# Performance work log

Hardware: AMD Instinct MI355X
Metric: run time of the kernel (lower is better)

Reference implementation:

```python
import jax, jax.numpy as jnp
import numpy as np

N_NODES = 50000
N_EDGES = 600000
N_REL = 8
D_IN = 128
D_OUT = 128


def setup_inputs() -> dict:
    key = jax.random.key(0)
    ks = jax.random.split(key, 12)
    s = 1.0 / np.sqrt(D_IN)
    s2 = 1.0 / np.sqrt(2 * D_IN)
    return {
        "x": jax.random.normal(ks[0], (N_NODES, D_IN), jnp.float32),
        "src": jax.random.randint(ks[1], (N_EDGES,), 0, N_NODES, jnp.int32),
        "dst": jax.random.randint(ks[2], (N_EDGES,), 0, N_NODES, jnp.int32),
        "etype": jax.random.randint(ks[3], (N_EDGES,), 0, N_REL, jnp.int32),
        "Wrel": jax.random.normal(ks[4], (N_REL, D_IN, D_OUT), jnp.float32) * s,
        "Wloop": jax.random.normal(ks[5], (D_IN, D_OUT), jnp.float32) * s,
        "brel": jax.random.normal(ks[6], (D_OUT,), jnp.float32) * s,
        "W1": jax.random.normal(ks[7], (2 * D_IN, 2 * D_IN), jnp.float32) * s2,
        "b1": jax.random.normal(ks[8], (2 * D_IN,), jnp.float32) * s2,
        "W2": jax.random.normal(ks[9], (2 * D_IN, D_OUT), jnp.float32) * s2,
        "b2": jax.random.normal(ks[10], (D_OUT,), jnp.float32) * s2,
    }


def rel_graph_conv(x, src, dst, etype, Wrel, Wloop, brel):
    # low_mem style: transform node features once per relation, then gather per edge.
    xW = jnp.einsum('ni,rio->rno', x, Wrel)          # [R, N, D_OUT]
    msg = xW[etype, src]                              # [E, D_OUT] gather by (rel, src)
    agg = jax.ops.segment_sum(msg, dst, num_segments=N_NODES)  # scatter-add to dst
    return agg + x @ Wloop + brel                     # self-loop + bias (DGL defaults)


def reference(x, src, dst, etype, Wrel, Wloop, brel, W1, b1, W2, b2):
    mid = rel_graph_conv(x, src, dst, etype, Wrel, Wloop, brel)
    h = jnp.concatenate([x, mid], axis=1)             # [N, 2*D_IN]
    h = jax.nn.relu(h @ W1 + b1)
    return h @ W2 + b2
```

## Files before the change

### kernel.cpp

```cpp
#include <hip/hip_runtime.h>

#define N_NODES 50000
#define N_EDGES 600000
#define N_REL 8
#define NT_PAD 50176
#define N_TILES 196

typedef __attribute__((ext_vector_type(8))) short bf16x8;
typedef __attribute__((ext_vector_type(4))) float f32x4;

__device__ __forceinline__ ushort f2b(float f) {
    union { float f; unsigned u; } v; v.f = f;
    unsigned r = v.u + 0x7FFFu + ((v.u >> 16) & 1u);
    return (ushort)(r >> 16);
}
__device__ __forceinline__ float b2f(ushort s) {
    union { unsigned u; float f; } v; v.u = ((unsigned)s) << 16;
    return v.f;
}


__global__ void conv_f32_bf16(const float* __restrict__ in, ushort* __restrict__ outb) {
    int i = (blockIdx.x * 256 + threadIdx.x) * 4;
    float4 f = *(const float4*)(in + i);
    ushort4 o; o.x = f2b(f.x); o.y = f2b(f.y); o.z = f2b(f.z); o.w = f2b(f.w);
    *(ushort4*)(outb + i) = o;
}

__global__ void transpose_wts3(const float* __restrict__ Wloop, const float* __restrict__ Wrel,
                               const float* __restrict__ W1, const float* __restrict__ W2,
                               ushort* __restrict__ wt) {
    int y = blockIdx.y;
    if (y == 0) {
        for (int idx = blockIdx.x * 256 + threadIdx.x; idx < 128 * 1152; idx += gridDim.x * 256) {
            int c = idx / 1152, kg = idx - c * 1152;
            float v = (kg < 1024) ? Wrel[(size_t)((kg >> 7) * 128 + (kg & 127)) * 128 + c]
                                  : Wloop[(size_t)(kg - 1024) * 128 + c];
            wt[idx] = f2b(v);
        }
    } else if (y == 1) {
        for (int idx = blockIdx.x * 256 + threadIdx.x; idx < 256 * 256; idx += gridDim.x * 256) {
            int c = idx >> 8, k = idx & 255;
            wt[147456 + idx] = f2b(W1[k * 256 + c]);
        }
    } else {
        for (int idx = blockIdx.x * 256 + threadIdx.x; idx < 128 * 256; idx += gridDim.x * 256) {
            int c = idx >> 8, k = idx & 255;
            wt[212992 + idx] = f2b(W2[k * 128 + c]);
        }
    }
}

template<int NPH, int KMODE, int AS, int CTOT, int OMODE>
__global__ __launch_bounds__(256) void mfma_gemm(
        const ushort* __restrict__ A0, const ushort* __restrict__ A1,
        const ushort* __restrict__ Bt, const float* __restrict__ bias,
        void* __restrict__ outv) {
    __shared__ ushort bs[128 * 136];
    const int t = threadIdx.x;
    const int wave = t >> 6, lane = t & 63;
    const int lr = lane & 15, lg = lane >> 4;
    const int wr = (wave >> 1) * 64, wc = (wave & 1) * 64;
    const int row0 = blockIdx.x * 128;
    const ushort* Btb = Bt + (size_t)blockIdx.y * 128 * (NPH * 128);

    f32x4 acc[4][4];
#pragma unroll
    for (int rt = 0; rt < 4; ++rt)
#pragma unroll
        for (int nt = 0; nt < 4; ++nt) acc[rt][nt] = (f32x4){0.f, 0.f, 0.f, 0.f};

#pragma unroll
    for (int p = 0; p < NPH; ++p) {
        const ushort* Ap; int as_;
        if (KMODE == 0) {
            if (p < 8) { Ap = A0 + p * 128; as_ = 1024; }
            else       { Ap = A1;           as_ = 128; }
        } else {
            Ap = p ? A1 : A0; as_ = AS;
        }
        bf16x8 af[4][4];
#pragma unroll
        for (int rt = 0; rt < 4; ++rt) {
            int ar = row0 + wr + rt * 16 + lr;
            if (ar >= N_NODES) ar = 0;
#pragma unroll
            for (int kc = 0; kc < 4; ++kc)
                af[rt][kc] = *(const bf16x8*)(Ap + (size_t)ar * as_ + kc * 32 + lg * 8);
        }
        if (p) __syncthreads();
#pragma unroll
        for (int it = 0; it < 8; ++it) {
            int idx = t + it * 256;
            int c = idx >> 4, gk = idx & 15;
            *(bf16x8*)(bs + c * 136 + gk * 8) =
                *(const bf16x8*)(Btb + (size_t)c * (NPH * 128) + p * 128 + gk * 8);
        }
        __syncthreads();
#pragma unroll
        for (int kc = 0; kc < 4; ++kc) {
            bf16x8 bf[4];
#pragma unroll
            for (int nt = 0; nt < 4; ++nt)
                bf[nt] = *(const bf16x8*)(bs + (wc + nt * 16 + lr) * 136 + kc * 32 + lg * 8);
#pragma unroll
            for (int rt = 0; rt < 4; ++rt)
#pragma unroll
                for (int nt = 0; nt < 4; ++nt)
                    acc[rt][nt] = __builtin_amdgcn_mfma_f32_16x16x32_bf16(af[rt][kc], bf[nt], acc[rt][nt], 0, 0, 0);
        }
    }

    const int colbase = blockIdx.y * 128;
#pragma unroll
    for (int rt = 0; rt < 4; ++rt) {
#pragma unroll
        for (int nt = 0; nt < 4; ++nt) {
            const int col = colbase + wc + nt * 16 + lr;
            const float bv = bias[col];
#pragma unroll
            for (int j = 0; j < 4; ++j) {
                const int r = row0 + wr + rt * 16 + lg * 4 + j;
                if (r >= N_NODES) continue;
                float vv = acc[rt][nt][j] + bv;
                if (OMODE == 0) {
                    ((float*)outv)[(size_t)r * CTOT + col] = vv;
                } else if (OMODE == 2) {
                    ((ushort*)outv)[(size_t)r * CTOT + col] = f2b(fmaxf(vv, 0.f));
                } else {
                    ((ushort*)outv)[(size_t)r * 128 + col] = f2b(vv);
                }
            }
        }
    }
}


__global__ void zero_cnt(int* __restrict__ cnt) {
    int i = blockIdx.x * 256 + threadIdx.x;
    if (i < NT_PAD) cnt[i] = 0;
}

__global__ void hist_dst(const int* __restrict__ dst, int* __restrict__ cnt) {
    int e = blockIdx.x * 256 + threadIdx.x;
    if (e < N_EDGES) atomicAdd(&cnt[dst[e]], 1);
}

__global__ void scan_tiles(const int* __restrict__ cnt, int* __restrict__ tincl, int* __restrict__ bsum) {
    __shared__ int s[256];
    int i = blockIdx.x * 256 + threadIdx.x;
    int v = cnt[i];
    s[threadIdx.x] = v;
    __syncthreads();
    for (int off = 1; off < 256; off <<= 1) {
        int add = (threadIdx.x >= off) ? s[threadIdx.x - off] : 0;
        __syncthreads();
        s[threadIdx.x] += add;
        __syncthreads();
    }
    tincl[i] = s[threadIdx.x];
    if (threadIdx.x == 255) bsum[blockIdx.x] = s[255];
}

__global__ void scan_bsum(const int* __restrict__ bsum, int* __restrict__ bex) {
    __shared__ int s[256];
    int v = (threadIdx.x < N_TILES) ? bsum[threadIdx.x] : 0;
    s[threadIdx.x] = v;
    __syncthreads();
    for (int off = 1; off < 256; off <<= 1) {
        int add = (threadIdx.x >= off) ? s[threadIdx.x - off] : 0;
        __syncthreads();
        s[threadIdx.x] += add;
        __syncthreads();
    }
    if (threadIdx.x < N_TILES) bex[threadIdx.x] = s[threadIdx.x] - v;
}

__global__ void finalize_base(const int* __restrict__ cnt, const int* __restrict__ tincl,
                              const int* __restrict__ bex, int* __restrict__ base,
                              int* __restrict__ cursor) {
    int i = blockIdx.x * 256 + threadIdx.x;
    int b = tincl[i] - cnt[i] + bex[blockIdx.x];
    base[i] = b; cursor[i] = b;
}

__global__ void scatter_ids(const int* __restrict__ src, const int* __restrict__ dst,
                            const int* __restrict__ et, int* __restrict__ cursor,
                            unsigned* __restrict__ sorted) {
    int e = blockIdx.x * 256 + threadIdx.x;
    if (e >= N_EDGES) return;
    int pos = atomicAdd(&cursor[dst[e]], 1);
    sorted[pos] = ((unsigned)src[e] << 3) | (unsigned)et[e];
}


__global__ __launch_bounds__(256) void gather_agg(
        const unsigned* __restrict__ sorted, const int* __restrict__ base,
        const int* __restrict__ cnt, const ushort* __restrict__ xbf,
        ushort* __restrict__ agg) {
    const int w = threadIdx.x >> 6, lane = threadIdx.x & 63;
    const int n = blockIdx.x * 4 + w;
    const int b = base[n], c = cnt[n];

    float a0[8], a1[8];
#pragma unroll
    for (int r = 0; r < 8; ++r) { a0[r] = 0.f; a1[r] = 0.f; }

    const unsigned* sp = sorted + b;
    int i = 0;
    for (; i + 4 <= c; i += 4) {
        unsigned d0 = sp[i], d1 = sp[i + 1], d2 = sp[i + 2], d3 = sp[i + 3];
        unsigned v0 = *(const unsigned*)(xbf + (size_t)(d0 >> 3) * 128 + lane * 2);
        unsigned v1 = *(const unsigned*)(xbf + (size_t)(d1 >> 3) * 128 + lane * 2);
        unsigned v2 = *(const unsigned*)(xbf + (size_t)(d2 >> 3) * 128 + lane * 2);
        unsigned v3 = *(const unsigned*)(xbf + (size_t)(d3 >> 3) * 128 + lane * 2);
#pragma unroll
        for (int r = 0; r < 8; ++r) {
            if ((d0 & 7u) == (unsigned)r) { a0[r] += b2f((ushort)(v0 & 0xffffu)); a1[r] += b2f((ushort)(v0 >> 16)); }
            if ((d1 & 7u) == (unsigned)r) { a0[r] += b2f((ushort)(v1 & 0xffffu)); a1[r] += b2f((ushort)(v1 >> 16)); }
            if ((d2 & 7u) == (unsigned)r) { a0[r] += b2f((ushort)(v2 & 0xffffu)); a1[r] += b2f((ushort)(v2 >> 16)); }
            if ((d3 & 7u) == (unsigned)r) { a0[r] += b2f((ushort)(v3 & 0xffffu)); a1[r] += b2f((ushort)(v3 >> 16)); }
        }
    }
    for (; i < c; ++i) {
        unsigned d = sp[i];
        unsigned v = *(const unsigned*)(xbf + (size_t)(d >> 3) * 128 + lane * 2);
#pragma unroll
        for (int r = 0; r < 8; ++r) {
            if ((d & 7u) == (unsigned)r) { a0[r] += b2f((ushort)(v & 0xffffu)); a1[r] += b2f((ushort)(v >> 16)); }
        }
    }
#pragma unroll
    for (int r = 0; r < 8; ++r) {
        unsigned pk = (unsigned)f2b(a0[r]) | ((unsigned)f2b(a1[r]) << 16);
        *(unsigned*)(agg + (size_t)n * 1024 + r * 128 + lane * 2) = pk;
    }
}


extern "C" void kernel_launch(void* const* d_in, const int* in_sizes, int n_in,
                              void* d_out, int out_size, void* d_ws, size_t ws_size,
                              hipStream_t stream) {
    const float* x     = (const float*)d_in[0];
    const int*   src   = (const int*)  d_in[1];
    const int*   dst   = (const int*)  d_in[2];
    const int*   etype = (const int*)  d_in[3];
    const float* Wrel  = (const float*)d_in[4];
    const float* Wloop = (const float*)d_in[5];
    const float* brel  = (const float*)d_in[6];
    const float* W1    = (const float*)d_in[7];
    const float* b1    = (const float*)d_in[8];
    const float* W2    = (const float*)d_in[9];
    const float* b2    = (const float*)d_in[10];
    float* out = (float*)d_out;

    char* ws = (char*)d_ws;
    ushort* agg   = (ushort*)ws;
    ushort* wt    = (ushort*)(ws + 102400000);
    char* meta    = ws + 102891520;
    int* cnt      = (int*)(meta);
    int* base     = (int*)(meta + 200704);
    int* cursor   = (int*)(meta + 401408);
    int* tincl    = (int*)(meta + 602112);
    int* bsum     = (int*)(meta + 802816);
    int* bex      = (int*)(meta + 803840);
    unsigned* sorted = (unsigned*)(meta + 804864);
    ushort* xbf   = (ushort*)(ws + 106096384);
    ushort* midbf = (ushort*)(ws + 118896384);

    const ushort* wst = wt;
    const ushort* w1t = wt + 147456;
    const ushort* w2t = wt + 212992;
    ushort* h = agg;

    conv_f32_bf16<<<6250, 256, 0, stream>>>(x, xbf);
    transpose_wts3<<<dim3(64, 3), 256, 0, stream>>>(Wloop, Wrel, W1, W2, wt);

    zero_cnt<<<N_TILES, 256, 0, stream>>>(cnt);
    hist_dst<<<(N_EDGES + 255) / 256, 256, 0, stream>>>(dst, cnt);
    scan_tiles<<<N_TILES, 256, 0, stream>>>(cnt, tincl, bsum);
    scan_bsum<<<1, 256, 0, stream>>>(bsum, bex);
    finalize_base<<<N_TILES, 256, 0, stream>>>(cnt, tincl, bex, base, cursor);
    scatter_ids<<<(N_EDGES + 255) / 256, 256, 0, stream>>>(src, dst, etype, cursor, sorted);

    gather_agg<<<N_NODES / 4, 256, 0, stream>>>(sorted, base, cnt, xbf, agg);

    mfma_gemm<9, 0, 0, 128, 4><<<dim3(391, 1), 256, 0, stream>>>(agg, xbf, wst, brel, (void*)midbf);

    mfma_gemm<2, 1, 128, 256, 2><<<dim3(391, 2), 256, 0, stream>>>(xbf, midbf, w1t, b1, (void*)h);

    mfma_gemm<2, 1, 256, 128, 0><<<dim3(391, 1), 256, 0, stream>>>(h, h + 128, w2t, b2, out);
}
```

Before: 236.0 us.

## Double-buffer B tiles and prefetch next-phase A fragments in MFMA GEMM

Restructures the GEMM K-loop into a software pipeline. The next phase's B tile and A fragments are loaded into registers while MFMAs run on the current phase, and the staged B goes into a second LDS buffer. The aim is to hide global-load latency and cut one barrier per phase. In exchange the kernel doubles LDS use and adds many registers (afn, sreg), with a launch_bounds occupancy hint of 2, which risks spills or lower occupancy.

```diff
diff --git a/kernel.cpp b/kernel.cpp
--- a/kernel.cpp
+++ b/kernel.cpp
@@ -52,17 +52,47 @@
 }
 
 template<int NPH, int KMODE, int AS, int CTOT, int OMODE>
-__global__ __launch_bounds__(256) void mfma_gemm(
+__global__ __launch_bounds__(256, 2) void mfma_gemm(
         const ushort* __restrict__ A0, const ushort* __restrict__ A1,
         const ushort* __restrict__ Bt, const float* __restrict__ bias,
         void* __restrict__ outv) {
-    __shared__ ushort bs[128 * 136];
+    __shared__ ushort bs[2][128 * 136];
     const int t = threadIdx.x;
     const int wave = t >> 6, lane = t & 63;
     const int lr = lane & 15, lg = lane >> 4;
     const int wr = (wave >> 1) * 64, wc = (wave & 1) * 64;
     const int row0 = blockIdx.x * 128;
     const ushort* Btb = Bt + (size_t)blockIdx.y * 128 * (NPH * 128);
+    const int sgk = (t & 15) * 8;
+    const int sc0 = t >> 4;
+
+#define STAGE_LOAD(p)                                                              \
+    _Pragma("unroll")                                                              \
+    for (int it = 0; it < 8; ++it)                                                 \
+        sreg[it] = *(const bf16x8*)(Btb + (size_t)(sc0 + it * 16) * (NPH * 128) +  \
+                                    (p) * 128 + sgk);
+
+#define STAGE_WRITE(b)                                                             \
+    _Pragma("unroll")                                                              \
+    for (int it = 0; it < 8; ++it)                                                 \
+        *(bf16x8*)(&bs[b][(sc0 + it * 16) * 136 + sgk]) = sreg[it];
+
+#define LOAD_AF(p, dstf)                                                           \
+    {                                                                              \
+        const ushort* Ap; int as_;                                                 \
+        if (KMODE == 0) {                                                          \
+            if ((p) < 8) { Ap = A0 + (p) * 128; as_ = 1024; }                      \
+            else         { Ap = A1;             as_ = 128;  }                      \
+        } else { Ap = (p) ? A1 : A0; as_ = AS; }                                   \
+        _Pragma("unroll")                                                          \
+        for (int rt = 0; rt < 4; ++rt) {                                           \
+            int ar = row0 + wr + rt * 16 + lr;                                     \
+            if (ar >= N_NODES) ar = 0;                                             \
+            _Pragma("unroll")                                                      \
+            for (int kc = 0; kc < 4; ++kc)                                         \
+                dstf[rt][kc] = *(const bf16x8*)(Ap + (size_t)ar * as_ + kc * 32 + lg * 8); \
+        }                                                                          \
+    }
 
     f32x4 acc[4][4];
 #pragma unroll
@@ -70,44 +100,41 @@
 #pragma unroll
         for (int nt = 0; nt < 4; ++nt) acc[rt][nt] = (f32x4){0.f, 0.f, 0.f, 0.f};
 
+    bf16x8 af[4][4], afn[4][4], sreg[8];
+
+    STAGE_LOAD(0);
+    LOAD_AF(0, af);
+    STAGE_WRITE(0);
+    __syncthreads();
+
 #pragma unroll
     for (int p = 0; p < NPH; ++p) {
-        const ushort* Ap; int as_;
-        if (KMODE == 0) {
-            if (p < 8) { Ap = A0 + p * 128; as_ = 1024; }
-            else       { Ap = A1;           as_ = 128; }
-        } else {
-            Ap = p ? A1 : A0; as_ = AS;
-        }
-        bf16x8 af[4][4];
-#pragma unroll
-        for (int rt = 0; rt < 4; ++rt) {
-            int ar = row0 + wr + rt * 16 + lr;
-            if (ar >= N_NODES) ar = 0;
-#pragma unroll
-            for (int kc = 0; kc < 4; ++kc)
-                af[rt][kc] = *(const bf16x8*)(Ap + (size_t)ar * as_ + kc * 32 + lg * 8);
-        }
-        if (p) __syncthreads();
-#pragma unroll
-        for (int it = 0; it < 8; ++it) {
-            int idx = t + it * 256;
-            int c = idx >> 4, gk = idx & 15;
-            *(bf16x8*)(bs + c * 136 + gk * 8) =
-                *(const bf16x8*)(Btb + (size_t)c * (NPH * 128) + p * 128 + gk * 8);
-        }
-        __syncthreads();
+        if (p + 1 < NPH) {
+            STAGE_LOAD(p + 1);
+            LOAD_AF(p + 1, afn);
+        }
+        const ushort* bcur = bs[p & 1];
 #pragma unroll
         for (int kc = 0; kc < 4; ++kc) {
             bf16x8 bf[4];
 #pragma unroll
             for (int nt = 0; nt < 4; ++nt)
-                bf[nt] = *(const bf16x8*)(bs + (wc + nt * 16 + lr) * 136 + kc * 32 + lg * 8);
+                bf[nt] = *(const bf16x8*)(bcur + (wc + nt * 16 + lr) * 136 + kc * 32 + lg * 8);
 #pragma unroll
             for (int rt = 0; rt < 4; ++rt)
 #pragma unroll
                 for (int nt = 0; nt < 4; ++nt)
                     acc[rt][nt] = __builtin_amdgcn_mfma_f32_16x16x32_bf16(af[rt][kc], bf[nt], acc[rt][nt], 0, 0, 0);
+        }
+        if (p + 1 < NPH) {
+            STAGE_WRITE((p + 1) & 1);
+        }
+        __syncthreads();
+        if (p + 1 < NPH) {
+#pragma unroll
+            for (int rt = 0; rt < 4; ++rt)
+#pragma unroll
+                for (int kc = 0; kc < 4; ++kc) af[rt][kc] = afn[rt][kc];
         }
     }
 
@@ -133,6 +160,9 @@
             }
         }
     }
+#undef STAGE_LOAD
+#undef STAGE_WRITE
+#undef LOAD_AF
 }
 
 
```

Measured after the change: 222.4 us. -5.8%, faster.
